# Performance work log

Measured on AMD Instinct MI355X. Metric: run time of the kernel, lower is better.

The kernel has to match this reference:

```python
import jax, jax.numpy as jnp
import numpy as np

INPUT_DIM = 41      # observed channels
D = 2 * INPUT_DIM   # attention value dim (values + mask concat)
E = 128             # embed_time
NH = 1              # num_heads
DK = E // NH
H = 128             # nhidden
NLIN = 50
LAT = 20
B, TK, TQ = 8, 512, 128


def _lin_init(k, out_d, in_d):
    return jax.random.normal(k, (out_d, in_d)) * (1.0 / np.sqrt(in_d))


def setup_inputs() -> dict:
    key = jax.random.key(0)
    ks = jax.random.split(key, 32)
    vals = jax.random.normal(ks[0], (B, TK, INPUT_DIM))
    obs = (jax.random.uniform(ks[1], (B, TK, INPUT_DIM)) > 0.3).astype(jnp.float32)
    x = jnp.concatenate([vals * obs, obs], axis=-1)          # [B,TK,2*INPUT_DIM]
    time_steps = jnp.sort(jax.random.uniform(ks[2], (B, TK)), axis=1)
    query = jnp.linspace(0.0, 1.0, TQ)                        # reference time points
    inp = dict(x=x, time_steps=time_steps, query=query)
    # learned time embedders (mtan_time_embedder): Linear(1,1) + Linear(1,E-1)
    inp['e1_wp'] = jax.random.normal(ks[3], (E - 1,)); inp['e1_bp'] = jax.random.normal(ks[4], (E - 1,)) * 0.1
    inp['e1_wl'] = jax.random.normal(ks[5], (1,));     inp['e1_bl'] = jax.random.normal(ks[6], (1,)) * 0.1
    inp['e2_wp'] = jax.random.normal(ks[7], (E - 1,)); inp['e2_bp'] = jax.random.normal(ks[8], (E - 1,)) * 0.1
    inp['e2_wl'] = jax.random.normal(ks[9], (1,));     inp['e2_bl'] = jax.random.normal(ks[10], (1,)) * 0.1
    # multiTimeAttention linears
    inp['Wq'] = _lin_init(ks[11], E, E); inp['bq'] = jnp.zeros((E,))
    inp['Wk'] = _lin_init(ks[12], E, E); inp['bk'] = jnp.zeros((E,))
    inp['Wo'] = _lin_init(ks[13], H, NH * D); inp['bo'] = jnp.zeros((H,))
    # bidirectional GRU (PyTorch layout: W_ih [3H,in], W_hh [3H,H])
    inp['gwi_f'] = _lin_init(ks[14], 3 * H, H); inp['gwh_f'] = _lin_init(ks[15], 3 * H, H)
    inp['gbi_f'] = jnp.zeros((3 * H,));         inp['gbh_f'] = jnp.zeros((3 * H,))
    inp['gwi_b'] = _lin_init(ks[16], 3 * H, H); inp['gwh_b'] = _lin_init(ks[17], 3 * H, H)
    inp['gbi_b'] = jnp.zeros((3 * H,));         inp['gbh_b'] = jnp.zeros((3 * H,))
    # hiddens_to_z0 MLP
    inp['W1'] = _lin_init(ks[18], NLIN, 2 * H); inp['b1'] = jnp.zeros((NLIN,))
    inp['W2'] = _lin_init(ks[19], 2 * LAT, NLIN); inp['b2'] = jnp.zeros((2 * LAT,))
    return inp


def _time_embed(tt, wp, bp, wl, bl):
    tt = tt[..., None]                               # [...,1]
    out1 = tt * wl + bl                              # [...,1]
    out2 = jnp.sin(tt * wp + bp)                     # [...,E-1]
    return jnp.concatenate([out1, out2], axis=-1)    # [...,E]


def _gru_scan(xs, Wi, Wh, bi, bh):
    # xs: [T,B,in] -> hidden states [T,B,H]; PyTorch GRU equations
    h0 = jnp.zeros((xs.shape[1], Wh.shape[1]), xs.dtype)
    def step(h, xt):
        gi = xt @ Wi.T + bi
        gh = h @ Wh.T + bh
        ir, iz, inn = jnp.split(gi, 3, axis=-1)
        hr, hz, hn = jnp.split(gh, 3, axis=-1)
        r = jax.nn.sigmoid(ir + hr)
        z = jax.nn.sigmoid(iz + hz)
        n = jnp.tanh(inn + r * hn)
        hnew = (1.0 - z) * n + z * h
        return hnew, hnew
    _, ys = jax.lax.scan(step, h0, xs)
    return ys


def reference(x, time_steps, query, e1_wp, e1_bp, e1_wl, e1_bl, e2_wp, e2_bp, e2_wl, e2_bl,
              Wq, bq, Wk, bk, Wo, bo, gwi_f, gwh_f, gbi_f, gbh_f, gwi_b, gwh_b, gbi_b, gbh_b,
              W1, b1, W2, b2):
    b, tk, _ = x.shape
    tq = query.shape[0]
    mask = x[:, :, INPUT_DIM:]                                 # [B,TK,INPUT_DIM]
    mask2 = jnp.concatenate([mask, mask], axis=-1)             # [B,TK,D]
    k_emb = _time_embed(time_steps, e1_wp, e1_bp, e1_wl, e1_bl)   # embedder1(key)   [B,TK,E]
    q_emb = _time_embed(query[None, :], e2_wp, e2_bp, e2_wl, e2_bl)  # embedder2(query) [1,TQ,E]
    q = (q_emb @ Wq.T + bq).reshape(1, tq, NH, DK).transpose(0, 2, 1, 3)   # [1,h,TQ,dk]
    k = (k_emb @ Wk.T + bk).reshape(b, tk, NH, DK).transpose(0, 2, 1, 3)   # [B,h,TK,dk]
    scores = jnp.einsum('ahqd,bhkd->bhqk', q, k) / np.sqrt(DK)             # [B,h,TQ,TK]
    # per-channel masked softmax over keys (the blown-up 5D tensor in the original)
    s5 = jnp.where(mask2[:, None, None, :, :] == 0, -1e9, scores[..., None])  # [B,h,TQ,TK,D]
    p = jax.nn.softmax(s5, axis=-2)
    att = jnp.einsum('bhqkd,bkd->bhqd', p, x)                  # value = x; [B,h,TQ,D]
    att = att.transpose(0, 2, 1, 3).reshape(b, tq, NH * D)
    out = att @ Wo.T + bo                                      # [B,TQ,H]
    xs = out.transpose(1, 0, 2)                                # [TQ,B,H]
    hf = _gru_scan(xs, gwi_f, gwh_f, gbi_f, gbh_f)
    hb = _gru_scan(xs[::-1], gwi_b, gwh_b, gbi_b, gbh_b)[::-1]
    h = jnp.concatenate([hf, hb], axis=-1).transpose(1, 0, 2)  # [B,TQ,2H]
    z = jax.nn.relu(h @ W1.T + b1) @ W2.T + b2                 # [B,TQ,2*LAT]
    return z
```

## Files before the change

kernel.cpp:

```cpp
#include <hip/hip_runtime.h>
#include <math.h>

#define TKK 512
#define TQQ 128
#define BB  8
#define EE  128
#define DD  82
#define IND 41
#define HH  128
#define G3  384
#define NL  50
#define OD  40

typedef __attribute__((ext_vector_type(8))) short short8v;
typedef __attribute__((ext_vector_type(4))) float f32x4;
#define MFMA16(a, b, c) __builtin_amdgcn_mfma_f32_16x16x32_bf16(a, b, c, 0, 0, 0)
#define RCP(x) __builtin_amdgcn_rcpf(x)

__device__ __forceinline__ short f2bf(float f) {
  unsigned u = __float_as_uint(f);
  unsigned r = (u + 0x7fffu + ((u >> 16) & 1u)) >> 16;
  return (short)r;
}
__device__ __forceinline__ float dot4(float4 a, float4 b) {
  return a.x * b.x + a.y * b.y + a.z * b.z + a.w * b.w;
}

__global__ __launch_bounds__(128) void embed_project(
    const float* __restrict__ time_steps, const float* __restrict__ query,
    const float* __restrict__ e1_wp, const float* __restrict__ e1_bp,
    const float* __restrict__ e1_wl, const float* __restrict__ e1_bl,
    const float* __restrict__ e2_wp, const float* __restrict__ e2_bp,
    const float* __restrict__ e2_wl, const float* __restrict__ e2_bl,
    const float* __restrict__ Wk, const float* __restrict__ bk,
    const float* __restrict__ Wq, const float* __restrict__ bq,
    float* __restrict__ kproj, float* __restrict__ qproj) {
  __shared__ float emb[8][EE];
  int i = blockIdx.x;
  int e = threadIdx.x;
  const float *wp, *bp, *wl, *bl, *W, *bias;
  float* out;
  int row0;
  const float* tsrc;
  if (i < 512) {
    int b = i & 7, rg = i >> 3;
    row0 = b * TKK + rg * 8;
    tsrc = time_steps + row0;
    wp = e1_wp; bp = e1_bp; wl = e1_wl; bl = e1_bl; W = Wk; bias = bk;
    out = kproj + (size_t)row0 * EE;
  } else {
    int qg = i - 512;
    row0 = qg * 8;
    tsrc = query + row0;
    wp = e2_wp; bp = e2_bp; wl = e2_wl; bl = e2_bl; W = Wq; bias = bq;
    out = qproj + (size_t)row0 * EE;
  }
  float wpv = 0.f, bpv = 0.f;
  if (e > 0) { wpv = wp[e - 1]; bpv = bp[e - 1]; }
  float wlv = wl[0], blv = bl[0];
#pragma unroll
  for (int r = 0; r < 8; r++) {
    float t = tsrc[r];
    emb[r][e] = (e == 0) ? (t * wlv + blv) : sinf(t * wpv + bpv);
  }
  __syncthreads();
  const float4* wr4 = (const float4*)(W + (size_t)e * EE);
  const float4* em4 = (const float4*)emb;
  float bv = bias[e];
  float acc[8];
#pragma unroll
  for (int r = 0; r < 8; r++) acc[r] = bv;
#pragma unroll 4
  for (int c = 0; c < 32; c++) {
    float4 wv = wr4[c];
#pragma unroll
    for (int r = 0; r < 8; r++) acc[r] += dot4(wv, em4[r * 32 + c]);
  }
#pragma unroll
  for (int r = 0; r < 8; r++) out[(size_t)r * EE + e] = acc[r];
}

__global__ __launch_bounds__(256) void attention(
    const float* __restrict__ x, const float* __restrict__ kproj,
    const float* __restrict__ qproj, const float* __restrict__ Wo,
    const float* __restrict__ bo,
    const float* __restrict__ gwi_f, const float* __restrict__ gbi_f,
    const float* __restrict__ gwi_b, const float* __restrict__ gbi_b,
    float* __restrict__ gi) {
  __shared__ float qv[4][EE];
  __shared__ float4 w4[TKK];
  __shared__ float red[4][4];
  __shared__ float mfin[4];
  __shared__ float part[2][4][DD];
  __shared__ float numb[4][DD];
  __shared__ float attb[4][DD];
  __shared__ float xsr[4][EE];
  int b = blockIdx.x & 7, qg = blockIdx.x >> 3;
  int q0 = qg * 4;
  int tid = threadIdx.x;

  {
    int idx = tid * 2, qi = idx >> 7, j = idx & 127;
    *(float2*)&qv[qi][j] = *(const float2*)(qproj + (size_t)(q0 + qi) * EE + j);
  }
  __syncthreads();

  float s0[4] = {0.f, 0.f, 0.f, 0.f}, s1[4] = {0.f, 0.f, 0.f, 0.f};
  {
    const float4* kr0 = (const float4*)(kproj + (size_t)(b * TKK + tid) * EE);
    const float4* kr1 = (const float4*)(kproj + (size_t)(b * TKK + 256 + tid) * EE);
    const float4* qv4 = (const float4*)qv;
#pragma unroll 8
    for (int c = 0; c < 32; c++) {
      float4 a0 = kr0[c], a1 = kr1[c];
#pragma unroll
      for (int qi = 0; qi < 4; qi++) {
        float4 cv = qv4[qi * 32 + c];
        s0[qi] += dot4(a0, cv);
        s1[qi] += dot4(a1, cv);
      }
    }
  }
  const float scale = 0.08838834764831845f;
  float lm[4];
#pragma unroll
  for (int qi = 0; qi < 4; qi++) {
    s0[qi] *= scale; s1[qi] *= scale;
    lm[qi] = fmaxf(s0[qi], s1[qi]);
  }
  for (int off = 32; off; off >>= 1)
#pragma unroll
    for (int qi = 0; qi < 4; qi++) lm[qi] = fmaxf(lm[qi], __shfl_xor(lm[qi], off, 64));
  if ((tid & 63) == 0)
#pragma unroll
    for (int qi = 0; qi < 4; qi++) red[tid >> 6][qi] = lm[qi];
  __syncthreads();
  if (tid < 4) {
    float m = red[0][tid];
    for (int w = 1; w < 4; w++) m = fmaxf(m, red[w][tid]);
    mfin[tid] = m;
  }
  __syncthreads();
  {
    float m0 = mfin[0], m1 = mfin[1], m2 = mfin[2], m3 = mfin[3];
    float4 e0, e1;
    e0.x = __expf(s0[0] - m0); e0.y = __expf(s0[1] - m1);
    e0.z = __expf(s0[2] - m2); e0.w = __expf(s0[3] - m3);
    e1.x = __expf(s1[0] - m0); e1.y = __expf(s1[1] - m1);
    e1.z = __expf(s1[2] - m2); e1.w = __expf(s1[3] - m3);
    w4[tid] = e0; w4[256 + tid] = e1;
  }
  __syncthreads();

  if (tid < 2 * DD) {
    int c = (tid >= DD), d = tid - c * DD;
    const float* xp = x + ((size_t)(b * TKK + c * 256)) * DD + d;
    float a0 = 0.f, a1 = 0.f, a2 = 0.f, a3 = 0.f;
#pragma unroll 8
    for (int k = 0; k < 256; k++) {
      float xv = xp[(size_t)k * DD];
      float4 wv = w4[c * 256 + k];
      a0 += wv.x * xv; a1 += wv.y * xv; a2 += wv.z * xv; a3 += wv.w * xv;
    }
    part[c][0][d] = a0; part[c][1][d] = a1; part[c][2][d] = a2; part[c][3][d] = a3;
  }
  __syncthreads();
  if (tid < DD) {
#pragma unroll
    for (int qi = 0; qi < 4; qi++) numb[qi][tid] = part[0][qi][tid] + part[1][qi][tid];
  }
  __syncthreads();
  if (tid < DD) {
    int j = tid % IND;
#pragma unroll
    for (int qi = 0; qi < 4; qi++)
      attb[qi][tid] = numb[qi][tid] * RCP(numb[qi][IND + j]);
  }
  __syncthreads();

  {
    int o = tid & 127, g = tid >> 7;
    const float* wo = Wo + (size_t)o * DD;
    float acc0 = bo[o], acc1 = acc0;
#pragma unroll 2
    for (int d = 0; d < DD; d++) {
      float wv = wo[d];
      acc0 += wv * attb[2 * g][d];
      acc1 += wv * attb[2 * g + 1][d];
    }
    xsr[2 * g][o] = acc0;
    xsr[2 * g + 1][o] = acc1;
  }
  __syncthreads();

  const float4* xs4 = (const float4*)xsr;
#pragma unroll
  for (int kk = 0; kk < 3; kk++) {
    int o = tid + kk * 256;
    int dirn = (o >= G3) ? 1 : 0;
    int oo = o - dirn * G3;
    int gate = oo >> 7, col = oo & 127;
    const float4* wr = (const float4*)((dirn ? gwi_b : gwi_f) + (size_t)oo * EE);
    float bi = (dirn ? gbi_b : gbi_f)[oo];
    float a0 = bi, a1 = bi, a2 = bi, a3 = bi;
#pragma unroll 4
    for (int c = 0; c < 32; c++) {
      float4 wv = wr[c];
      a0 += dot4(wv, xs4[0 * 32 + c]);
      a1 += dot4(wv, xs4[1 * 32 + c]);
      a2 += dot4(wv, xs4[2 * 32 + c]);
      a3 += dot4(wv, xs4[3 * 32 + c]);
    }
    float* gp = gi + (((size_t)(dirn * BB + b) * TQQ + q0) * HH + col) * 4 + gate;
    gp[0] = a0; gp[512] = a1; gp[1024] = a2; gp[1536] = a3;
  }
}

__global__ __launch_bounds__(512, 1) void gru_seq(const float* __restrict__ gi,
                                                  const float* __restrict__ gwh_f,
                                                  const float* __restrict__ gbh_f,
                                                  const float* __restrict__ gwh_b,
                                                  const float* __restrict__ gbh_b,
                                                  float* __restrict__ hcat) {
  __shared__ short hb[2][HH];
  int dir = blockIdx.x >> 3, b = blockIdx.x & 7;
  const float* Wh = dir ? gwh_b : gwh_f;
  const float* bh = dir ? gbh_b : gbh_f;
  int tid = threadIdx.x;
  int w = tid >> 6, l = tid & 63;
  int lhi = l >> 4, llo = l & 15;
  int o = 16 * w + llo;
  bool tl = (lhi == 0);

  for (int i = tid; i < 2 * HH / 2; i += 512) ((int*)hb)[i] = 0;

  short8v Bf[3][4];
#pragma unroll
  for (int g = 0; g < 3; g++) {
    const float* wr = Wh + (size_t)(g * HH + o) * EE;
#pragma unroll
    for (int kk = 0; kk < 4; kk++) {
      int k0 = kk * 32 + lhi * 8;
      short8v v;
#pragma unroll
      for (int i = 0; i < 8; i++) v[i] = f2bf(wr[k0 + i]);
      Bf[g][kk] = v;
    }
  }
  float bhr = bh[o], bhz = bh[HH + o], bhn = bh[2 * HH + o];
  float hprev = 0.f;
  float hst[16];

  float4 g0, g1, g2, g3;
  const size_t dbase = ((size_t)(dir * BB + b) * TQQ) * 512 + (size_t)o * 4;

  auto gi_load = [&](int step, float4& dst) {
    int tt = dir ? (TQQ - 1 - step) : step;
    dst = *(const float4*)(gi + dbase + (size_t)tt * 512);
  };
  __syncthreads();
  gi_load(0, g0); gi_load(1, g1);

  auto body = [&](int step, float4& gc, float4& gn, float& hs) {
    int cur = step & 1;
    const char* hrow = (const char*)&hb[cur][0];
    int ao = lhi * 16;
    short8v A0 = *(const short8v*)(hrow + 0 * 64 + ao);
    short8v A1 = *(const short8v*)(hrow + 1 * 64 + ao);
    short8v A2 = *(const short8v*)(hrow + 2 * 64 + ao);
    short8v A3 = *(const short8v*)(hrow + 3 * 64 + ao);
    { int ls = step + 2; gi_load(ls > TQQ - 1 ? TQQ - 1 : ls, gn); }
    f32x4 z4 = {0.f, 0.f, 0.f, 0.f};
    f32x4 aR = z4, aZ = z4, aN = z4;
    aR = MFMA16(A0, Bf[0][0], aR); aZ = MFMA16(A0, Bf[1][0], aZ); aN = MFMA16(A0, Bf[2][0], aN);
    aR = MFMA16(A1, Bf[0][1], aR); aZ = MFMA16(A1, Bf[1][1], aZ); aN = MFMA16(A1, Bf[2][1], aN);
    aR = MFMA16(A2, Bf[0][2], aR); aZ = MFMA16(A2, Bf[1][2], aZ); aN = MFMA16(A2, Bf[2][2], aN);
    aR = MFMA16(A3, Bf[0][3], aR); aZ = MFMA16(A3, Bf[1][3], aZ); aN = MFMA16(A3, Bf[2][3], aN);
    if (tl) {
      float rp = gc.x + bhr + aR[0];
      float zp = gc.y + bhz + aZ[0];
      float hn = aN[0] + bhn;
      float r = RCP(1.f + __expf(-rp));
      float z = RCP(1.f + __expf(-zp));
      float a = gc.z + r * hn;
      float e = __expf(2.f * a);
      float n = 1.f - 2.f * RCP(1.f + e);
      float hnew = n + z * (hprev - n);
      hprev = hnew;
      hs = hnew;
      hb[cur ^ 1][o] = f2bf(hnew);
    }
    asm volatile("s_waitcnt lgkmcnt(0)" ::: "memory");
    __builtin_amdgcn_s_barrier();
    __builtin_amdgcn_sched_barrier(0);
  };

  for (int so = 0; so < TQQ / 16; so++) {
    int s0i = so * 16;
    body(s0i + 0,  g0, g2, hst[0]);
    body(s0i + 1,  g1, g3, hst[1]);
    body(s0i + 2,  g2, g0, hst[2]);
    body(s0i + 3,  g3, g1, hst[3]);
    body(s0i + 4,  g0, g2, hst[4]);
    body(s0i + 5,  g1, g3, hst[5]);
    body(s0i + 6,  g2, g0, hst[6]);
    body(s0i + 7,  g3, g1, hst[7]);
    body(s0i + 8,  g0, g2, hst[8]);
    body(s0i + 9,  g1, g3, hst[9]);
    body(s0i + 10, g2, g0, hst[10]);
    body(s0i + 11, g3, g1, hst[11]);
    body(s0i + 12, g0, g2, hst[12]);
    body(s0i + 13, g1, g3, hst[13]);
    body(s0i + 14, g2, g0, hst[14]);
    body(s0i + 15, g3, g1, hst[15]);
    if (tl) {
#pragma unroll
      for (int si = 0; si < 16; si++) {
        int step = s0i + si;
        int t = dir ? (TQQ - 1 - step) : step;
        hcat[((size_t)b * TQQ + t) * (2 * HH) + dir * HH + o] = hst[si];
      }
    }
  }
}

__global__ __launch_bounds__(512) void mlp_out(const float* __restrict__ hcat,
                                               const float* __restrict__ W1,
                                               const float* __restrict__ b1,
                                               const float* __restrict__ W2,
                                               const float* __restrict__ b2,
                                               float* __restrict__ out) {
  __shared__ float hrow[8][2 * HH];
  __shared__ float ybuf[8][52];
  int i = blockIdx.x;
  int b = i & 7, tg = i >> 3;
  int tid = threadIdx.x;
  size_t rowbase = (size_t)(b * TQQ + tg * 8) * (2 * HH);
  ((float4*)hrow)[tid] = *(const float4*)(hcat + rowbase + tid * 4);
  __syncthreads();
  int r = tid >> 6, o = tid & 63;
  if (o < NL) {
    const float4* w1 = (const float4*)(W1 + (size_t)o * (2 * HH));
    const float4* h4 = (const float4*)hrow[r];
    float acc = b1[o];
#pragma unroll 8
    for (int c = 0; c < 64; c++) acc += dot4(w1[c], h4[c]);
    ybuf[r][o] = fmaxf(acc, 0.f);
  }
  __syncthreads();
  if (o < OD) {
    const float* w2 = W2 + (size_t)o * NL;
    float acc = b2[o];
#pragma unroll 10
    for (int j = 0; j < NL; j++) acc += w2[j] * ybuf[r][j];
    out[((size_t)(b * TQQ + tg * 8) + r) * OD + o] = acc;
  }
}

extern "C" void kernel_launch(void* const* d_in, const int* in_sizes, int n_in,
                              void* d_out, int out_size, void* d_ws, size_t ws_size,
                              hipStream_t stream) {
  const float* x          = (const float*)d_in[0];
  const float* time_steps = (const float*)d_in[1];
  const float* query      = (const float*)d_in[2];
  const float* e1_wp = (const float*)d_in[3];
  const float* e1_bp = (const float*)d_in[4];
  const float* e1_wl = (const float*)d_in[5];
  const float* e1_bl = (const float*)d_in[6];
  const float* e2_wp = (const float*)d_in[7];
  const float* e2_bp = (const float*)d_in[8];
  const float* e2_wl = (const float*)d_in[9];
  const float* e2_bl = (const float*)d_in[10];
  const float* Wq = (const float*)d_in[11];
  const float* bq = (const float*)d_in[12];
  const float* Wk = (const float*)d_in[13];
  const float* bk = (const float*)d_in[14];
  const float* Wo = (const float*)d_in[15];
  const float* bo = (const float*)d_in[16];
  const float* gwi_f = (const float*)d_in[17];
  const float* gwh_f = (const float*)d_in[18];
  const float* gbi_f = (const float*)d_in[19];
  const float* gbh_f = (const float*)d_in[20];
  const float* gwi_b = (const float*)d_in[21];
  const float* gwh_b = (const float*)d_in[22];
  const float* gbi_b = (const float*)d_in[23];
  const float* gbh_b = (const float*)d_in[24];
  const float* W1 = (const float*)d_in[25];
  const float* b1 = (const float*)d_in[26];
  const float* W2 = (const float*)d_in[27];
  const float* b2 = (const float*)d_in[28];

  float* ws    = (float*)d_ws;
  float* kproj = ws;
  float* qproj = kproj + 4096 * 128;
  float* gi    = qproj + 128 * 128;
  float* hcat  = gi + 16 * 128 * 128 * 4;

  embed_project<<<528, 128, 0, stream>>>(time_steps, query,
                                         e1_wp, e1_bp, e1_wl, e1_bl,
                                         e2_wp, e2_bp, e2_wl, e2_bl,
                                         Wk, bk, Wq, bq, kproj, qproj);
  attention<<<256, 256, 0, stream>>>(x, kproj, qproj, Wo, bo,
                                     gwi_f, gbi_f, gwi_b, gbi_b, gi);
  gru_seq<<<16, 512, 0, stream>>>(gi, gwh_f, gbh_f, gwh_b, gbh_b, hcat);
  mlp_out<<<128, 512, 0, stream>>>(hcat, W1, b1, W2, b2, (float*)d_out);
}
```

Measured before the change: 113.4 us.

## Fuse attention and GRU into one kernel with per-tile flag handoff

Merges the attention/input-projection kernel and the sequential GRU kernel into a single launch. The first 16 blocks run the GRU recurrence and spin on per-(batch, query-tile) atomic flags that the remaining 256 attention blocks set after writing their gi slices, so the recurrence can start before all attention work finishes. Attention blocks are widened to 512 threads, each handling one key instead of two. This removes a kernel boundary and overlaps the serial GRU with attention, but adds a memset, spin-wait polling, and depends on all blocks being co-resident to avoid deadlock.

```diff
diff --git a/kernel.cpp b/kernel.cpp
--- a/kernel.cpp
+++ b/kernel.cpp
@@ -80,247 +80,249 @@
   for (int r = 0; r < 8; r++) out[(size_t)r * EE + e] = acc[r];
 }
 
-__global__ __launch_bounds__(256) void attention(
+__global__ __launch_bounds__(512) void attn_gru(
     const float* __restrict__ x, const float* __restrict__ kproj,
     const float* __restrict__ qproj, const float* __restrict__ Wo,
     const float* __restrict__ bo,
     const float* __restrict__ gwi_f, const float* __restrict__ gbi_f,
     const float* __restrict__ gwi_b, const float* __restrict__ gbi_b,
-    float* __restrict__ gi) {
-  __shared__ float qv[4][EE];
-  __shared__ float4 w4[TKK];
-  __shared__ float red[4][4];
-  __shared__ float mfin[4];
-  __shared__ float part[2][4][DD];
-  __shared__ float numb[4][DD];
-  __shared__ float attb[4][DD];
-  __shared__ float xsr[4][EE];
-  int b = blockIdx.x & 7, qg = blockIdx.x >> 3;
-  int q0 = qg * 4;
-  int tid = threadIdx.x;
-
-  {
-    int idx = tid * 2, qi = idx >> 7, j = idx & 127;
-    *(float2*)&qv[qi][j] = *(const float2*)(qproj + (size_t)(q0 + qi) * EE + j);
-  }
-  __syncthreads();
-
-  float s0[4] = {0.f, 0.f, 0.f, 0.f}, s1[4] = {0.f, 0.f, 0.f, 0.f};
-  {
-    const float4* kr0 = (const float4*)(kproj + (size_t)(b * TKK + tid) * EE);
-    const float4* kr1 = (const float4*)(kproj + (size_t)(b * TKK + 256 + tid) * EE);
-    const float4* qv4 = (const float4*)qv;
+    const float* __restrict__ gwh_f, const float* __restrict__ gbh_f,
+    const float* __restrict__ gwh_b, const float* __restrict__ gbh_b,
+    float* __restrict__ gi, float* __restrict__ hcat, int* flags) {
+  int bid = blockIdx.x;
+  if (bid < 16) {
+    __shared__ short hb[2][HH];
+    int dir = bid >> 3, b = bid & 7;
+    const float* Wh = dir ? gwh_b : gwh_f;
+    const float* bh = dir ? gbh_b : gbh_f;
+    int tid = threadIdx.x;
+    int w = tid >> 6, l = tid & 63;
+    int lhi = l >> 4, llo = l & 15;
+    int o = 16 * w + llo;
+    bool tl = (lhi == 0);
+
+    if (tid < HH) { hb[0][tid] = 0; hb[1][tid] = 0; }
+
+    short8v Bf[3][4];
+#pragma unroll
+    for (int g = 0; g < 3; g++) {
+      const float* wr = Wh + (size_t)(g * HH + o) * EE;
+#pragma unroll
+      for (int kk = 0; kk < 4; kk++) {
+        int k0 = kk * 32 + lhi * 8;
+        short8v v;
+#pragma unroll
+        for (int i = 0; i < 8; i++) v[i] = f2bf(wr[k0 + i]);
+        Bf[g][kk] = v;
+      }
+    }
+    float bhr = bh[o], bhz = bh[HH + o], bhn = bh[2 * HH + o];
+    float hprev = 0.f;
+    float hst[16];
+
+    float4 g0, g1, g2, g3;
+    const size_t dbase = ((size_t)(dir * BB + b) * TQQ) * 512 + (size_t)o * 4;
+
+    auto gi_load = [&](int step, float4& dst) {
+      int tt = dir ? (TQQ - 1 - step) : step;
+      dst = *(const float4*)(gi + dbase + (size_t)tt * 512);
+    };
+    auto spin_tile = [&](int so_) {
+      int soc = so_ > 31 ? 31 : so_;
+      int tile = dir ? (31 - soc) : soc;
+      const int* fp = flags + b * 32 + tile;
+      while (__hip_atomic_load(fp, __ATOMIC_ACQUIRE, __HIP_MEMORY_SCOPE_AGENT) == 0)
+        __builtin_amdgcn_s_sleep(2);
+    };
+    __syncthreads();
+    spin_tile(0);
+    gi_load(0, g0); gi_load(1, g1);
+
+    auto body = [&](int step, float4& gc, float4& gn, float& hs) {
+      int cur = step & 1;
+      const char* hrow = (const char*)&hb[cur][0];
+      int ao = lhi * 16;
+      short8v A0 = *(const short8v*)(hrow + 0 * 64 + ao);
+      short8v A1 = *(const short8v*)(hrow + 1 * 64 + ao);
+      short8v A2 = *(const short8v*)(hrow + 2 * 64 + ao);
+      short8v A3 = *(const short8v*)(hrow + 3 * 64 + ao);
+      { int ls = step + 2; gi_load(ls > TQQ - 1 ? TQQ - 1 : ls, gn); }
+      f32x4 z4 = {0.f, 0.f, 0.f, 0.f};
+      f32x4 aR = z4, aZ = z4, aN = z4;
+      aR = MFMA16(A0, Bf[0][0], aR); aZ = MFMA16(A0, Bf[1][0], aZ); aN = MFMA16(A0, Bf[2][0], aN);
+      aR = MFMA16(A1, Bf[0][1], aR); aZ = MFMA16(A1, Bf[1][1], aZ); aN = MFMA16(A1, Bf[2][1], aN);
+      aR = MFMA16(A2, Bf[0][2], aR); aZ = MFMA16(A2, Bf[1][2], aZ); aN = MFMA16(A2, Bf[2][2], aN);
+      aR = MFMA16(A3, Bf[0][3], aR); aZ = MFMA16(A3, Bf[1][3], aZ); aN = MFMA16(A3, Bf[2][3], aN);
+      if (tl) {
+        float rp = gc.x + bhr + aR[0];
+        float zp = gc.y + bhz + aZ[0];
+        float hn = aN[0] + bhn;
+        float r = RCP(1.f + __expf(-rp));
+        float z = RCP(1.f + __expf(-zp));
+        float a = gc.z + r * hn;
+        float e = __expf(2.f * a);
+        float n = 1.f - 2.f * RCP(1.f + e);
+        float hnew = n + z * (hprev - n);
+        hprev = hnew;
+        hs = hnew;
+        hb[cur ^ 1][o] = f2bf(hnew);
+      }
+      asm volatile("s_waitcnt lgkmcnt(0)" ::: "memory");
+      __builtin_amdgcn_s_barrier();
+      __builtin_amdgcn_sched_barrier(0);
+    };
+
+    for (int grp = 0; grp < 8; grp++) {
+      int s0i = grp * 16;
+      spin_tile(4 * grp + 1);
+      body(s0i + 0,  g0, g2, hst[0]);
+      body(s0i + 1,  g1, g3, hst[1]);
+      body(s0i + 2,  g2, g0, hst[2]);
+      body(s0i + 3,  g3, g1, hst[3]);
+      spin_tile(4 * grp + 2);
+      body(s0i + 4,  g0, g2, hst[4]);
+      body(s0i + 5,  g1, g3, hst[5]);
+      body(s0i + 6,  g2, g0, hst[6]);
+      body(s0i + 7,  g3, g1, hst[7]);
+      spin_tile(4 * grp + 3);
+      body(s0i + 8,  g0, g2, hst[8]);
+      body(s0i + 9,  g1, g3, hst[9]);
+      body(s0i + 10, g2, g0, hst[10]);
+      body(s0i + 11, g3, g1, hst[11]);
+      spin_tile(4 * grp + 4);
+      body(s0i + 12, g0, g2, hst[12]);
+      body(s0i + 13, g1, g3, hst[13]);
+      body(s0i + 14, g2, g0, hst[14]);
+      body(s0i + 15, g3, g1, hst[15]);
+      if (tl) {
+#pragma unroll
+        for (int si = 0; si < 16; si++) {
+          int step = s0i + si;
+          int t = dir ? (TQQ - 1 - step) : step;
+          hcat[((size_t)b * TQQ + t) * (2 * HH) + dir * HH + o] = hst[si];
+        }
+      }
+    }
+  } else {
+    __shared__ float qv[4][EE];
+    __shared__ float4 w4[TKK];
+    __shared__ float red[8][4];
+    __shared__ float mfin[4];
+    __shared__ float part[4][4][DD];
+    __shared__ float numb[4][DD];
+    __shared__ float attb[4][DD];
+    __shared__ float xsr[4][EE];
+    int j = bid - 16;
+    int b = j & 7, qg = j >> 3;
+    int q0 = qg * 4;
+    int tid = threadIdx.x;
+
+    qv[tid >> 7][tid & 127] = qproj[(size_t)(q0 + (tid >> 7)) * EE + (tid & 127)];
+    __syncthreads();
+
+    float s[4] = {0.f, 0.f, 0.f, 0.f};
+    {
+      const float4* kr = (const float4*)(kproj + (size_t)(b * TKK + tid) * EE);
+      const float4* qv4 = (const float4*)qv;
 #pragma unroll 8
-    for (int c = 0; c < 32; c++) {
-      float4 a0 = kr0[c], a1 = kr1[c];
-#pragma unroll
-      for (int qi = 0; qi < 4; qi++) {
-        float4 cv = qv4[qi * 32 + c];
-        s0[qi] += dot4(a0, cv);
-        s1[qi] += dot4(a1, cv);
-      }
-    }
-  }
-  const float scale = 0.08838834764831845f;
-  float lm[4];
-#pragma unroll
-  for (int qi = 0; qi < 4; qi++) {
-    s0[qi] *= scale; s1[qi] *= scale;
-    lm[qi] = fmaxf(s0[qi], s1[qi]);
-  }
-  for (int off = 32; off; off >>= 1)
-#pragma unroll
-    for (int qi = 0; qi < 4; qi++) lm[qi] = fmaxf(lm[qi], __shfl_xor(lm[qi], off, 64));
-  if ((tid & 63) == 0)
-#pragma unroll
-    for (int qi = 0; qi < 4; qi++) red[tid >> 6][qi] = lm[qi];
-  __syncthreads();
-  if (tid < 4) {
-    float m = red[0][tid];
-    for (int w = 1; w < 4; w++) m = fmaxf(m, red[w][tid]);
-    mfin[tid] = m;
-  }
-  __syncthreads();
-  {
-    float m0 = mfin[0], m1 = mfin[1], m2 = mfin[2], m3 = mfin[3];
-    float4 e0, e1;
-    e0.x = __expf(s0[0] - m0); e0.y = __expf(s0[1] - m1);
-    e0.z = __expf(s0[2] - m2); e0.w = __expf(s0[3] - m3);
-    e1.x = __expf(s1[0] - m0); e1.y = __expf(s1[1] - m1);
-    e1.z = __expf(s1[2] - m2); e1.w = __expf(s1[3] - m3);
-    w4[tid] = e0; w4[256 + tid] = e1;
-  }
-  __syncthreads();
-
-  if (tid < 2 * DD) {
-    int c = (tid >= DD), d = tid - c * DD;
-    const float* xp = x + ((size_t)(b * TKK + c * 256)) * DD + d;
-    float a0 = 0.f, a1 = 0.f, a2 = 0.f, a3 = 0.f;
+      for (int c = 0; c < 32; c++) {
+        float4 a = kr[c];
+#pragma unroll
+        for (int qi = 0; qi < 4; qi++) s[qi] += dot4(a, qv4[qi * 32 + c]);
+      }
+    }
+    const float scale = 0.08838834764831845f;
+    float lm[4];
+#pragma unroll
+    for (int qi = 0; qi < 4; qi++) { s[qi] *= scale; lm[qi] = s[qi]; }
+    for (int off = 32; off; off >>= 1)
+#pragma unroll
+      for (int qi = 0; qi < 4; qi++) lm[qi] = fmaxf(lm[qi], __shfl_xor(lm[qi], off, 64));
+    if ((tid & 63) == 0)
+#pragma unroll
+      for (int qi = 0; qi < 4; qi++) red[tid >> 6][qi] = lm[qi];
+    __syncthreads();
+    if (tid < 4) {
+      float m = red[0][tid];
+#pragma unroll
+      for (int w = 1; w < 8; w++) m = fmaxf(m, red[w][tid]);
+      mfin[tid] = m;
+    }
+    __syncthreads();
+    {
+      float4 e0;
+      e0.x = __expf(s[0] - mfin[0]); e0.y = __expf(s[1] - mfin[1]);
+      e0.z = __expf(s[2] - mfin[2]); e0.w = __expf(s[3] - mfin[3]);
+      w4[tid] = e0;
+    }
+    __syncthreads();
+
+    {
+      int c2 = tid >> 7, d = tid & 127;
+      if (d < DD) {
+        const float* xp = x + ((size_t)(b * TKK + c2 * 128)) * DD + d;
+        float a0 = 0.f, a1 = 0.f, a2 = 0.f, a3 = 0.f;
 #pragma unroll 8
-    for (int k = 0; k < 256; k++) {
-      float xv = xp[(size_t)k * DD];
-      float4 wv = w4[c * 256 + k];
-      a0 += wv.x * xv; a1 += wv.y * xv; a2 += wv.z * xv; a3 += wv.w * xv;
-    }
-    part[c][0][d] = a0; part[c][1][d] = a1; part[c][2][d] = a2; part[c][3][d] = a3;
-  }
-  __syncthreads();
-  if (tid < DD) {
-#pragma unroll
-    for (int qi = 0; qi < 4; qi++) numb[qi][tid] = part[0][qi][tid] + part[1][qi][tid];
-  }
-  __syncthreads();
-  if (tid < DD) {
-    int j = tid % IND;
-#pragma unroll
-    for (int qi = 0; qi < 4; qi++)
-      attb[qi][tid] = numb[qi][tid] * RCP(numb[qi][IND + j]);
-  }
-  __syncthreads();
-
-  {
-    int o = tid & 127, g = tid >> 7;
-    const float* wo = Wo + (size_t)o * DD;
-    float acc0 = bo[o], acc1 = acc0;
+        for (int k = 0; k < 128; k++) {
+          float xv = xp[(size_t)k * DD];
+          float4 wv = w4[c2 * 128 + k];
+          a0 += wv.x * xv; a1 += wv.y * xv; a2 += wv.z * xv; a3 += wv.w * xv;
+        }
+        part[c2][0][d] = a0; part[c2][1][d] = a1; part[c2][2][d] = a2; part[c2][3][d] = a3;
+      }
+    }
+    __syncthreads();
+    if (tid < DD) {
+#pragma unroll
+      for (int qi = 0; qi < 4; qi++)
+        numb[qi][tid] = part[0][qi][tid] + part[1][qi][tid] + part[2][qi][tid] + part[3][qi][tid];
+    }
+    __syncthreads();
+    if (tid < DD) {
+      int jj = tid % IND;
+#pragma unroll
+      for (int qi = 0; qi < 4; qi++)
+        attb[qi][tid] = numb[qi][tid] * RCP(numb[qi][IND + jj]);
+    }
+    __syncthreads();
+
+    {
+      int o = tid & 127, g = tid >> 7;
+      const float* wo = Wo + (size_t)o * DD;
+      float acc = bo[o];
 #pragma unroll 2
-    for (int d = 0; d < DD; d++) {
-      float wv = wo[d];
-      acc0 += wv * attb[2 * g][d];
-      acc1 += wv * attb[2 * g + 1][d];
-    }
-    xsr[2 * g][o] = acc0;
-    xsr[2 * g + 1][o] = acc1;
-  }
-  __syncthreads();
-
-  const float4* xs4 = (const float4*)xsr;
-#pragma unroll
-  for (int kk = 0; kk < 3; kk++) {
-    int o = tid + kk * 256;
-    int dirn = (o >= G3) ? 1 : 0;
-    int oo = o - dirn * G3;
-    int gate = oo >> 7, col = oo & 127;
-    const float4* wr = (const float4*)((dirn ? gwi_b : gwi_f) + (size_t)oo * EE);
-    float bi = (dirn ? gbi_b : gbi_f)[oo];
-    float a0 = bi, a1 = bi, a2 = bi, a3 = bi;
+      for (int d = 0; d < DD; d++) acc += wo[d] * attb[g][d];
+      xsr[g][o] = acc;
+    }
+    __syncthreads();
+
+    const float4* xs4 = (const float4*)xsr;
+#pragma unroll
+    for (int kk = 0; kk < 2; kk++) {
+      int o = tid + kk * 512;
+      if (o < 2 * G3) {
+        int dirn = (o >= G3) ? 1 : 0;
+        int oo = o - dirn * G3;
+        int gate = oo >> 7, col = oo & 127;
+        const float4* wr = (const float4*)((dirn ? gwi_b : gwi_f) + (size_t)oo * EE);
+        float bi = (dirn ? gbi_b : gbi_f)[oo];
+        float a0 = bi, a1 = bi, a2 = bi, a3 = bi;
 #pragma unroll 4
-    for (int c = 0; c < 32; c++) {
-      float4 wv = wr[c];
-      a0 += dot4(wv, xs4[0 * 32 + c]);
-      a1 += dot4(wv, xs4[1 * 32 + c]);
-      a2 += dot4(wv, xs4[2 * 32 + c]);
-      a3 += dot4(wv, xs4[3 * 32 + c]);
-    }
-    float* gp = gi + (((size_t)(dirn * BB + b) * TQQ + q0) * HH + col) * 4 + gate;
-    gp[0] = a0; gp[512] = a1; gp[1024] = a2; gp[1536] = a3;
-  }
-}
-
-__global__ __launch_bounds__(512, 1) void gru_seq(const float* __restrict__ gi,
-                                                  const float* __restrict__ gwh_f,
-                                                  const float* __restrict__ gbh_f,
-                                                  const float* __restrict__ gwh_b,
-                                                  const float* __restrict__ gbh_b,
-                                                  float* __restrict__ hcat) {
-  __shared__ short hb[2][HH];
-  int dir = blockIdx.x >> 3, b = blockIdx.x & 7;
-  const float* Wh = dir ? gwh_b : gwh_f;
-  const float* bh = dir ? gbh_b : gbh_f;
-  int tid = threadIdx.x;
-  int w = tid >> 6, l = tid & 63;
-  int lhi = l >> 4, llo = l & 15;
-  int o = 16 * w + llo;
-  bool tl = (lhi == 0);
-
-  for (int i = tid; i < 2 * HH / 2; i += 512) ((int*)hb)[i] = 0;
-
-  short8v Bf[3][4];
-#pragma unroll
-  for (int g = 0; g < 3; g++) {
-    const float* wr = Wh + (size_t)(g * HH + o) * EE;
-#pragma unroll
-    for (int kk = 0; kk < 4; kk++) {
-      int k0 = kk * 32 + lhi * 8;
-      short8v v;
-#pragma unroll
-      for (int i = 0; i < 8; i++) v[i] = f2bf(wr[k0 + i]);
-      Bf[g][kk] = v;
-    }
-  }
-  float bhr = bh[o], bhz = bh[HH + o], bhn = bh[2 * HH + o];
-  float hprev = 0.f;
-  float hst[16];
-
-  float4 g0, g1, g2, g3;
-  const size_t dbase = ((size_t)(dir * BB + b) * TQQ) * 512 + (size_t)o * 4;
-
-  auto gi_load = [&](int step, float4& dst) {
-    int tt = dir ? (TQQ - 1 - step) : step;
-    dst = *(const float4*)(gi + dbase + (size_t)tt * 512);
-  };
-  __syncthreads();
-  gi_load(0, g0); gi_load(1, g1);
-
-  auto body = [&](int step, float4& gc, float4& gn, float& hs) {
-    int cur = step & 1;
-    const char* hrow = (const char*)&hb[cur][0];
-    int ao = lhi * 16;
-    short8v A0 = *(const short8v*)(hrow + 0 * 64 + ao);
-    short8v A1 = *(const short8v*)(hrow + 1 * 64 + ao);
-    short8v A2 = *(const short8v*)(hrow + 2 * 64 + ao);
-    short8v A3 = *(const short8v*)(hrow + 3 * 64 + ao);
-    { int ls = step + 2; gi_load(ls > TQQ - 1 ? TQQ - 1 : ls, gn); }
-    f32x4 z4 = {0.f, 0.f, 0.f, 0.f};
-    f32x4 aR = z4, aZ = z4, aN = z4;
-    aR = MFMA16(A0, Bf[0][0], aR); aZ = MFMA16(A0, Bf[1][0], aZ); aN = MFMA16(A0, Bf[2][0], aN);
-    aR = MFMA16(A1, Bf[0][1], aR); aZ = MFMA16(A1, Bf[1][1], aZ); aN = MFMA16(A1, Bf[2][1], aN);
-    aR = MFMA16(A2, Bf[0][2], aR); aZ = MFMA16(A2, Bf[1][2], aZ); aN = MFMA16(A2, Bf[2][2], aN);
-    aR = MFMA16(A3, Bf[0][3], aR); aZ = MFMA16(A3, Bf[1][3], aZ); aN = MFMA16(A3, Bf[2][3], aN);
-    if (tl) {
-      float rp = gc.x + bhr + aR[0];
-      float zp = gc.y + bhz + aZ[0];
-      float hn = aN[0] + bhn;
-      float r = RCP(1.f + __expf(-rp));
-      float z = RCP(1.f + __expf(-zp));
-      float a = gc.z + r * hn;
-      float e = __expf(2.f * a);
-      float n = 1.f - 2.f * RCP(1.f + e);
-      float hnew = n + z * (hprev - n);
-      hprev = hnew;
-      hs = hnew;
-      hb[cur ^ 1][o] = f2bf(hnew);
-    }
-    asm volatile("s_waitcnt lgkmcnt(0)" ::: "memory");
-    __builtin_amdgcn_s_barrier();
-    __builtin_amdgcn_sched_barrier(0);
-  };
-
-  for (int so = 0; so < TQQ / 16; so++) {
-    int s0i = so * 16;
-    body(s0i + 0,  g0, g2, hst[0]);
-    body(s0i + 1,  g1, g3, hst[1]);
-    body(s0i + 2,  g2, g0, hst[2]);
-    body(s0i + 3,  g3, g1, hst[3]);
-    body(s0i + 4,  g0, g2, hst[4]);
-    body(s0i + 5,  g1, g3, hst[5]);
-    body(s0i + 6,  g2, g0, hst[6]);
-    body(s0i + 7,  g3, g1, hst[7]);
-    body(s0i + 8,  g0, g2, hst[8]);
-    body(s0i + 9,  g1, g3, hst[9]);
-    body(s0i + 10, g2, g0, hst[10]);
-    body(s0i + 11, g3, g1, hst[11]);
-    body(s0i + 12, g0, g2, hst[12]);
-    body(s0i + 13, g1, g3, hst[13]);
-    body(s0i + 14, g2, g0, hst[14]);
-    body(s0i + 15, g3, g1, hst[15]);
-    if (tl) {
-#pragma unroll
-      for (int si = 0; si < 16; si++) {
-        int step = s0i + si;
-        int t = dir ? (TQQ - 1 - step) : step;
-        hcat[((size_t)b * TQQ + t) * (2 * HH) + dir * HH + o] = hst[si];
-      }
-    }
+        for (int c = 0; c < 32; c++) {
+          float4 wv = wr[c];
+          a0 += dot4(wv, xs4[0 * 32 + c]);
+          a1 += dot4(wv, xs4[1 * 32 + c]);
+          a2 += dot4(wv, xs4[2 * 32 + c]);
+          a3 += dot4(wv, xs4[3 * 32 + c]);
+        }
+        float* gp = gi + (((size_t)(dirn * BB + b) * TQQ + q0) * HH + col) * 4 + gate;
+        gp[0] = a0; gp[512] = a1; gp[1024] = a2; gp[1536] = a3;
+      }
+    }
+    __threadfence();
+    __syncthreads();
+    if (tid == 0)
+      __hip_atomic_fetch_add(&flags[b * 32 + qg], 1, __ATOMIC_RELEASE, __HIP_MEMORY_SCOPE_AGENT);
   }
 }
 
@@ -395,13 +397,16 @@
   float* qproj = kproj + 4096 * 128;
   float* gi    = qproj + 128 * 128;
   float* hcat  = gi + 16 * 128 * 128 * 4;
-
+  int*   flags = (int*)(hcat + 8 * 128 * 256);
+
+  hipMemsetAsync(flags, 0, 8 * 32 * sizeof(int), stream);
   embed_project<<<528, 128, 0, stream>>>(time_steps, query,
                                          e1_wp, e1_bp, e1_wl, e1_bl,
                                          e2_wp, e2_bp, e2_wl, e2_bl,
                                          Wk, bk, Wq, bq, kproj, qproj);
-  attention<<<256, 256, 0, stream>>>(x, kproj, qproj, Wo, bo,
-                                     gwi_f, gbi_f, gwi_b, gbi_b, gi);
-  gru_seq<<<16, 512, 0, stream>>>(gi, gwh_f, gbh_f, gwh_b, gbh_b, hcat);
+  attn_gru<<<272, 512, 0, stream>>>(x, kproj, qproj, Wo, bo,
+                                    gwi_f, gbi_f, gwi_b, gbi_b,
+                                    gwh_f, gbh_f, gwh_b, gbh_b,
+                                    gi, hcat, flags);
   mlp_out<<<128, 512, 0, stream>>>(hcat, W1, b1, W2, b2, (float*)d_out);
 }
```

New measurement: 227.4 us. 101% more time.

## Coalesce key and GRU-input weight reads with quad-split rows; stage Wo in LDS

Applied to the files above, without the earlier changes.

The score computation and the GRU input projection now give each row to four adjacent lanes, each reading interleaved float4 chunks, and combine the partial sums with shuffles. Before, each thread streamed a whole 512-byte row on its own, so global loads were badly uncoalesced. Raw scores are staged in LDS and exponentiated after the max reduction, and the Wo matrix (about 42 KB) is copied cooperatively into shared memory before the output projection. The extra LDS lowers occupancy, and the shuffles and row loops add instructions.

```diff
diff --git a/kernel.cpp b/kernel.cpp
--- a/kernel.cpp
+++ b/kernel.cpp
@@ -95,38 +95,46 @@
   __shared__ float numb[4][DD];
   __shared__ float attb[4][DD];
   __shared__ float xsr[4][EE];
+  __shared__ float wo_lds[HH * DD];
   int b = blockIdx.x & 7, qg = blockIdx.x >> 3;
   int q0 = qg * 4;
   int tid = threadIdx.x;
+  int rq = tid >> 2, ec = tid & 3;
 
   {
     int idx = tid * 2, qi = idx >> 7, j = idx & 127;
     *(float2*)&qv[qi][j] = *(const float2*)(qproj + (size_t)(q0 + qi) * EE + j);
-  }
-  __syncthreads();
-
-  float s0[4] = {0.f, 0.f, 0.f, 0.f}, s1[4] = {0.f, 0.f, 0.f, 0.f};
-  {
-    const float4* kr0 = (const float4*)(kproj + (size_t)(b * TKK + tid) * EE);
-    const float4* kr1 = (const float4*)(kproj + (size_t)(b * TKK + 256 + tid) * EE);
-    const float4* qv4 = (const float4*)qv;
-#pragma unroll 8
-    for (int c = 0; c < 32; c++) {
-      float4 a0 = kr0[c], a1 = kr1[c];
-#pragma unroll
-      for (int qi = 0; qi < 4; qi++) {
-        float4 cv = qv4[qi * 32 + c];
-        s0[qi] += dot4(a0, cv);
-        s1[qi] += dot4(a1, cv);
-      }
-    }
-  }
+    const float4* wo4 = (const float4*)Wo;
+    float4* wl4 = (float4*)wo_lds;
+#pragma unroll
+    for (int it = 0; it < 11; it++) {
+      int i4 = tid + it * 256;
+      if (i4 < HH * DD / 4) wl4[i4] = wo4[i4];
+    }
+  }
+  __syncthreads();
+
   const float scale = 0.08838834764831845f;
-  float lm[4];
-#pragma unroll
-  for (int qi = 0; qi < 4; qi++) {
-    s0[qi] *= scale; s1[qi] *= scale;
-    lm[qi] = fmaxf(s0[qi], s1[qi]);
+  float lm[4] = {-1e30f, -1e30f, -1e30f, -1e30f};
+  const float4* qv4 = (const float4*)qv;
+  for (int p = 0; p < 8; p++) {
+    int r = p * 64 + rq;
+    const float4* kr = (const float4*)(kproj + (size_t)(b * TKK + r) * EE);
+    float s[4] = {0.f, 0.f, 0.f, 0.f};
+#pragma unroll
+    for (int c = 0; c < 8; c++) {
+      float4 kv = kr[c * 4 + ec];
+#pragma unroll
+      for (int qi = 0; qi < 4; qi++) s[qi] += dot4(kv, qv4[qi * 32 + c * 4 + ec]);
+    }
+#pragma unroll
+    for (int qi = 0; qi < 4; qi++) {
+      s[qi] += __shfl_xor(s[qi], 1, 64);
+      s[qi] += __shfl_xor(s[qi], 2, 64);
+      s[qi] *= scale;
+      lm[qi] = fmaxf(lm[qi], s[qi]);
+    }
+    if (ec == 0) { float4 sv = {s[0], s[1], s[2], s[3]}; w4[r] = sv; }
   }
   for (int off = 32; off; off >>= 1)
 #pragma unroll
@@ -143,12 +151,12 @@
   __syncthreads();
   {
     float m0 = mfin[0], m1 = mfin[1], m2 = mfin[2], m3 = mfin[3];
-    float4 e0, e1;
-    e0.x = __expf(s0[0] - m0); e0.y = __expf(s0[1] - m1);
-    e0.z = __expf(s0[2] - m2); e0.w = __expf(s0[3] - m3);
-    e1.x = __expf(s1[0] - m0); e1.y = __expf(s1[1] - m1);
-    e1.z = __expf(s1[2] - m2); e1.w = __expf(s1[3] - m3);
-    w4[tid] = e0; w4[256 + tid] = e1;
+    float4 v0 = w4[tid], v1 = w4[256 + tid];
+    v0.x = __expf(v0.x - m0); v0.y = __expf(v0.y - m1);
+    v0.z = __expf(v0.z - m2); v0.w = __expf(v0.w - m3);
+    v1.x = __expf(v1.x - m0); v1.y = __expf(v1.y - m1);
+    v1.z = __expf(v1.z - m2); v1.w = __expf(v1.w - m3);
+    w4[tid] = v0; w4[256 + tid] = v1;
   }
   __syncthreads();
 
@@ -180,11 +188,11 @@
 
   {
     int o = tid & 127, g = tid >> 7;
-    const float* wo = Wo + (size_t)o * DD;
+    const float* wrow = wo_lds + o * DD;
     float acc0 = bo[o], acc1 = acc0;
 #pragma unroll 2
     for (int d = 0; d < DD; d++) {
-      float wv = wo[d];
+      float wv = wrow[d];
       acc0 += wv * attb[2 * g][d];
       acc1 += wv * attb[2 * g + 1][d];
     }
@@ -194,25 +202,29 @@
   __syncthreads();
 
   const float4* xs4 = (const float4*)xsr;
-#pragma unroll
-  for (int kk = 0; kk < 3; kk++) {
-    int o = tid + kk * 256;
+  for (int p = 0; p < 12; p++) {
+    int o = p * 64 + rq;
     int dirn = (o >= G3) ? 1 : 0;
     int oo = o - dirn * G3;
     int gate = oo >> 7, col = oo & 127;
     const float4* wr = (const float4*)((dirn ? gwi_b : gwi_f) + (size_t)oo * EE);
+    float a[4] = {0.f, 0.f, 0.f, 0.f};
+#pragma unroll
+    for (int c = 0; c < 8; c++) {
+      float4 wv = wr[c * 4 + ec];
+#pragma unroll
+      for (int qi = 0; qi < 4; qi++) a[qi] += dot4(wv, xs4[qi * 32 + c * 4 + ec]);
+    }
+#pragma unroll
+    for (int qi = 0; qi < 4; qi++) {
+      a[qi] += __shfl_xor(a[qi], 1, 64);
+      a[qi] += __shfl_xor(a[qi], 2, 64);
+    }
     float bi = (dirn ? gbi_b : gbi_f)[oo];
-    float a0 = bi, a1 = bi, a2 = bi, a3 = bi;
-#pragma unroll 4
-    for (int c = 0; c < 32; c++) {
-      float4 wv = wr[c];
-      a0 += dot4(wv, xs4[0 * 32 + c]);
-      a1 += dot4(wv, xs4[1 * 32 + c]);
-      a2 += dot4(wv, xs4[2 * 32 + c]);
-      a3 += dot4(wv, xs4[3 * 32 + c]);
-    }
-    float* gp = gi + (((size_t)(dirn * BB + b) * TQQ + q0) * HH + col) * 4 + gate;
-    gp[0] = a0; gp[512] = a1; gp[1024] = a2; gp[1536] = a3;
+    if (ec == 0) {
+      float* gp = gi + (((size_t)(dirn * BB + b) * TQQ + q0) * HH + col) * 4 + gate;
+      gp[0] = a[0] + bi; gp[512] = a[1] + bi; gp[1024] = a[2] + bi; gp[1536] = a[3] + bi;
+    }
   }
 }
 
```

Result: faster. 104.8 us (-7.6%).
